# Kernel tuning notes

Measured on AMD Instinct MI355X. Metric: run time of the kernel, lower is better.

The kernel has to match this reference:

```python
import jax, jax.numpy as jnp
import numpy as np

N_NODES = 50000
N_EDGES = 600000
D = 128
EDGE_D = 32
N_LAYERS = 3
BN_EPS = 1e-5


def setup_inputs() -> dict:
    key = jax.random.key(0)
    ks = jax.random.split(key, 8)
    x = jax.random.normal(ks[0], (N_NODES, D), dtype=jnp.float32)
    edge_index = jax.random.randint(ks[1], (2, N_EDGES), 0, N_NODES, dtype=jnp.int64)
    edge_attr = jax.random.normal(ks[2], (N_EDGES, EDGE_D), dtype=jnp.float32)
    W_lin = jax.random.normal(ks[3], (N_LAYERS, EDGE_D, D), dtype=jnp.float32) * 0.05
    b_lin = jnp.zeros((N_LAYERS, D), dtype=jnp.float32)
    W1 = jax.random.normal(ks[4], (N_LAYERS, D, D), dtype=jnp.float32) * 0.05
    b1 = jnp.zeros((N_LAYERS, D), dtype=jnp.float32)
    W2 = jax.random.normal(ks[5], (N_LAYERS, D, D), dtype=jnp.float32) * 0.05
    b2 = jnp.zeros((N_LAYERS, D), dtype=jnp.float32)
    gamma = jnp.ones((N_LAYERS, D), dtype=jnp.float32)
    beta = jnp.zeros((N_LAYERS, D), dtype=jnp.float32)
    return {"x": x, "edge_index": edge_index, "edge_attr": edge_attr,
            "W_lin": W_lin, "b_lin": b_lin, "W1": W1, "b1": b1,
            "W2": W2, "b2": b2, "gamma": gamma, "beta": beta}


def reference(x, edge_index, edge_attr, W_lin, b_lin, W1, b1, W2, b2, gamma, beta):
    # MPNN with GINEConv layers: for each layer,
    #   msg_e = ReLU(x[src_e] + Linear(edge_attr_e))      (PyG GINEConv edge lift)
    #   agg_i = sum over edges with dst==i of msg_e        (scatter-sum)
    #   h     = MLP((1+eps)*x + agg), eps=0
    #   x     = ReLU(BatchNorm1d(h))                       (training-mode batch stats)
    src, dst = edge_index[0], edge_index[1]
    n = x.shape[0]
    for l in range(W1.shape[0]):
        e = edge_attr @ W_lin[l] + b_lin[l]                 # [E, D]
        msg = jax.nn.relu(x[src] + e)                       # gather + fuse
        agg = jax.ops.segment_sum(msg, dst, num_segments=n)  # [N, D]
        h = x + agg                                         # eps = 0
        h = jax.nn.relu(h @ W1[l] + b1[l]) @ W2[l] + b2[l]   # GIN MLP
        mu = jnp.mean(h, axis=0)
        var = jnp.var(h, axis=0)
        h = (h - mu) * jax.lax.rsqrt(var + BN_EPS) * gamma[l] + beta[l]
        x = jax.nn.relu(h)
    return x
```

## Files before the change

### kernel.cpp

```cpp
#include <hip/hip_runtime.h>

#define D_DIM 128
#define EDGE_DIM 32
#define BN_EPS 1e-5f

typedef __attribute__((ext_vector_type(8))) _Float16 f16x8;
typedef __attribute__((ext_vector_type(2))) _Float16 half2v;
typedef __attribute__((ext_vector_type(4))) float f32x4;
typedef unsigned short ushort_t;

__device__ __forceinline__ unsigned short f2h(float f) {
    union { _Float16 h; unsigned short u; } c;
    c.h = (_Float16)f;
    return c.u;
}
__device__ __forceinline__ unsigned pk2h(float lo, float hi) {
    return (unsigned)f2h(lo) | ((unsigned)f2h(hi) << 16);
}
__device__ __forceinline__ half2v asH2(unsigned u) {
    union { unsigned u; half2v h; } c;
    c.u = u;
    return c.h;
}
__device__ __forceinline__ float fdot2f(half2v a, half2v b, float c) {
#if __has_builtin(__builtin_amdgcn_fdot2)
    return __builtin_amdgcn_fdot2(a, b, c, false);
#else
    return c + (float)a.x * (float)b.x + (float)a.y * (float)b.y;
#endif
}

__global__ __launch_bounds__(256) void hist_kernel(
    const int* __restrict__ dst, int* __restrict__ cnt, int E)
{
    for (int e = blockIdx.x * 256 + threadIdx.x; e < E; e += gridDim.x * 256)
        atomicAdd(&cnt[dst[e]], 1);
}

__global__ __launch_bounds__(256) void scan_local_kernel(
    const int* __restrict__ cnt, int* __restrict__ off,
    int* __restrict__ blksum, int n)
{
    __shared__ int part[256];
    const int t = threadIdx.x;
    const int base = blockIdx.x * 2048 + t * 8;
    int v[8];
    int s = 0;
#pragma unroll
    for (int j = 0; j < 8; ++j) {
        const int idx = base + j;
        const int c = (idx < n) ? cnt[idx] : 0;
        v[j] = s;
        s += c;
    }
    part[t] = s;
    __syncthreads();
    for (int d = 1; d < 256; d <<= 1) {
        const int val = (t >= d) ? part[t - d] : 0;
        __syncthreads();
        part[t] += val;
        __syncthreads();
    }
    const int texcl = (t > 0) ? part[t - 1] : 0;
#pragma unroll
    for (int j = 0; j < 8; ++j) {
        const int idx = base + j;
        if (idx < n) off[idx] = texcl + v[j];
    }
    if (t == 255) blksum[blockIdx.x] = part[255];
}

__global__ __launch_bounds__(64) void scan_tops_kernel(
    int* __restrict__ blksum, int* __restrict__ off, int n, int B)
{
    if (threadIdx.x == 0) {
        int run = 0;
        for (int b = 0; b < B; ++b) {
            const int v = blksum[b];
            blksum[b] = run;
            run += v;
        }
        off[n] = run;
    }
}

__global__ __launch_bounds__(256) void scan_add_kernel(
    int* __restrict__ off, int* __restrict__ cur,
    const int* __restrict__ blksum, int n)
{
    const int base = blockIdx.x * 2048;
    const int add = blksum[blockIdx.x];
    for (int j = threadIdx.x; j < 2048; j += 256) {
        const int i = base + j;
        if (i < n) {
            const int v = off[i] + add;
            off[i] = v;
            cur[i] = v;
        }
    }
}

__global__ __launch_bounds__(256) void scatter_conv_kernel(
    const int* __restrict__ src, const int* __restrict__ dst,
    const float* __restrict__ ea,
    int* __restrict__ cur, int* __restrict__ srcs,
    uint4* __restrict__ ea16q, int E)
{
    for (int e = blockIdx.x * 256 + threadIdx.x; e < E; e += gridDim.x * 256) {
        const int p = atomicAdd(&cur[dst[e]], 1);
        srcs[p] = src[e];
        const float* __restrict__ er = ea + (size_t)e * EDGE_DIM;
#pragma unroll
        for (int q = 0; q < 4; ++q) {
            const float4 a = *(const float4*)(er + q * 8);
            const float4 b = *(const float4*)(er + q * 8 + 4);
            uint4 o;
            o.x = pk2h(a.x, a.y); o.y = pk2h(a.z, a.w);
            o.z = pk2h(b.x, b.y); o.w = pk2h(b.z, b.w);
            ea16q[(size_t)p * 4 + q] = o;
        }
    }
}

__global__ __launch_bounds__(256) void wbuild_kernel(
    const float* __restrict__ Wl, const float* __restrict__ W1f,
    const float* __restrict__ W2f,
    unsigned* __restrict__ wl16d, unsigned* __restrict__ wf1d,
    unsigned* __restrict__ wf2d)
{
    const int idx = blockIdx.x * 256 + threadIdx.x;
    if (idx < 2048) {
        const int kp = idx >> 7, c = idx & 127;
        wl16d[idx] = pk2h(Wl[(2 * kp) * D_DIM + c], Wl[(2 * kp + 1) * D_DIM + c]);
    } else if (idx < 10240) {
        const int i = idx - 2048;
        const int col = i >> 6, kp = i & 63;
        wf1d[i] = pk2h(W1f[(2 * kp) * D_DIM + col], W1f[(2 * kp + 1) * D_DIM + col]);
    } else if (idx < 18432) {
        const int i = idx - 10240;
        const int col = i >> 6, kp = i & 63;
        wf2d[i] = pk2h(W2f[(2 * kp) * D_DIM + col], W2f[(2 * kp + 1) * D_DIM + col]);
    }
}

__global__ __launch_bounds__(256) void xprep0_kernel(
    const float* __restrict__ h, uint2* __restrict__ x16q, int M)
{
    const int total = M * 32;
    for (int i = blockIdx.x * 256 + threadIdx.x; i < total; i += gridDim.x * 256) {
        const float4 v = ((const float4*)h)[i];
        uint2 o; o.x = pk2h(v.x, v.y); o.y = pk2h(v.z, v.w);
        x16q[i] = o;
    }
}

template<int OUTF32>
__global__ __launch_bounds__(256) void apply_kernel(
    const ushort_t* __restrict__ h16, const float* __restrict__ scsh,
    uint2* __restrict__ x16q, float* __restrict__ outp, int M)
{
    __shared__ float sc[128], sh[128];
    if (threadIdx.x < 128) {
        sc[threadIdx.x] = scsh[threadIdx.x];
        sh[threadIdx.x] = scsh[128 + threadIdx.x];
    }
    __syncthreads();
    const int total = M * 32;
    for (int i = blockIdx.x * 256 + threadIdx.x; i < total; i += gridDim.x * 256) {
        const uint2 hv = *(const uint2*)(h16 + (size_t)i * 4);
        const half2v a = asH2(hv.x), b = asH2(hv.y);
        const int c = (i & 31) * 4;
        const float v0 = fmaxf(fmaf((float)a.x, sc[c + 0], sh[c + 0]), 0.f);
        const float v1 = fmaxf(fmaf((float)a.y, sc[c + 1], sh[c + 1]), 0.f);
        const float v2 = fmaxf(fmaf((float)b.x, sc[c + 2], sh[c + 2]), 0.f);
        const float v3 = fmaxf(fmaf((float)b.y, sc[c + 3], sh[c + 3]), 0.f);
        if (OUTF32) {
            f32x4 o = {v0, v1, v2, v3};
            *(f32x4*)(outp + (size_t)i * 4) = o;
        } else {
            uint2 o; o.x = pk2h(v0, v1); o.y = pk2h(v2, v3);
            x16q[i] = o;
        }
    }
}

__global__ __launch_bounds__(256, 2) void edge_agg_kernel(
    const unsigned* __restrict__ x16d,
    const int*      __restrict__ srcs,
    const uint4*    __restrict__ ea16q,
    const int*      __restrict__ row_off,
    const unsigned* __restrict__ wl16d,
    const float*    __restrict__ bl,
    unsigned*       __restrict__ agg16d,
    int nNodes)
{
    const int lane = threadIdx.x & 63;
    const int wid  = threadIdx.x >> 6;

    unsigned wA[16], wB[16];
#pragma unroll
    for (int kp = 0; kp < 16; ++kp) {
        const uint2 w2 = *(const uint2*)(wl16d + kp * 128 + 2 * lane);
        wA[kp] = w2.x; wB[kp] = w2.y;
    }
#pragma unroll
    for (int kp = 0; kp < 16; ++kp) {
        asm volatile("" : "+v"(wA[kp]));
        asm volatile("" : "+v"(wB[kp]));
    }
    const float b0 = bl[2 * lane];
    const float b1 = bl[2 * lane + 1];

    const int stride = gridDim.x * 4;
    for (int node = blockIdx.x * 4 + wid; node < nNodes; node += stride) {
        const int beg = __builtin_amdgcn_readfirstlane(row_off[node]);
        const int end = __builtin_amdgcn_readfirstlane(row_off[node + 1]);
        float acc0 = 0.f, acc1 = 0.f;

        const int nPair = (end - beg) >> 1;
        int j = beg;
        int sA = 0, sB = 0;
        if (nPair > 0) { sA = srcs[j]; sB = srcs[j + 1]; }

#pragma unroll 1
        for (int it = 0; it < nPair; ++it) {
            const unsigned xdA = x16d[(size_t)sA * 64 + lane];
            const unsigned xdB = x16d[(size_t)sB * 64 + lane];
            int sA2 = sA, sB2 = sB;
            if (it + 1 < nPair) {
                sA2 = srcs[j + 2];
                sB2 = srcs[j + 3];
            }
            const uint4 a0 = ea16q[(size_t)j * 4 + 0];
            const uint4 a1 = ea16q[(size_t)j * 4 + 1];
            const uint4 a2 = ea16q[(size_t)j * 4 + 2];
            const uint4 a3 = ea16q[(size_t)j * 4 + 3];
            const uint4 c0 = ea16q[(size_t)(j + 1) * 4 + 0];
            const uint4 c1 = ea16q[(size_t)(j + 1) * 4 + 1];
            const uint4 c2 = ea16q[(size_t)(j + 1) * 4 + 2];
            const uint4 c3 = ea16q[(size_t)(j + 1) * 4 + 3];

            const unsigned awA[16] = {a0.x, a0.y, a0.z, a0.w,
                                      a1.x, a1.y, a1.z, a1.w,
                                      a2.x, a2.y, a2.z, a2.w,
                                      a3.x, a3.y, a3.z, a3.w};
            const unsigned awB[16] = {c0.x, c0.y, c0.z, c0.w,
                                      c1.x, c1.y, c1.z, c1.w,
                                      c2.x, c2.y, c2.z, c2.w,
                                      c3.x, c3.y, c3.z, c3.w};
            float pA0 = b0, pA1 = b1, pB0 = b0, pB1 = b1;
            float qA0 = 0.f, qA1 = 0.f, qB0 = 0.f, qB1 = 0.f;
#pragma unroll
            for (int kp = 0; kp < 8; ++kp) {
                pA0 = fdot2f(asH2(awA[kp]), asH2(wA[kp]), pA0);
                pA1 = fdot2f(asH2(awA[kp]), asH2(wB[kp]), pA1);
                pB0 = fdot2f(asH2(awB[kp]), asH2(wA[kp]), pB0);
                pB1 = fdot2f(asH2(awB[kp]), asH2(wB[kp]), pB1);
                qA0 = fdot2f(asH2(awA[kp + 8]), asH2(wA[kp + 8]), qA0);
                qA1 = fdot2f(asH2(awA[kp + 8]), asH2(wB[kp + 8]), qA1);
                qB0 = fdot2f(asH2(awB[kp + 8]), asH2(wA[kp + 8]), qB0);
                qB1 = fdot2f(asH2(awB[kp + 8]), asH2(wB[kp + 8]), qB1);
            }
            const half2v xhA = asH2(xdA);
            const half2v xhB = asH2(xdB);
            acc0 += fmaxf((float)xhA.x + pA0 + qA0, 0.f)
                  + fmaxf((float)xhB.x + pB0 + qB0, 0.f);
            acc1 += fmaxf((float)xhA.y + pA1 + qA1, 0.f)
                  + fmaxf((float)xhB.y + pB1 + qB1, 0.f);
            sA = sA2; sB = sB2;
            j += 2;
        }
        if (j < end) {
            const int s = srcs[j];
            const unsigned xd = x16d[(size_t)s * 64 + lane];
            const uint4 a0 = ea16q[(size_t)j * 4 + 0];
            const uint4 a1 = ea16q[(size_t)j * 4 + 1];
            const uint4 a2 = ea16q[(size_t)j * 4 + 2];
            const uint4 a3 = ea16q[(size_t)j * 4 + 3];
            const unsigned aw[16] = {a0.x, a0.y, a0.z, a0.w,
                                     a1.x, a1.y, a1.z, a1.w,
                                     a2.x, a2.y, a2.z, a2.w,
                                     a3.x, a3.y, a3.z, a3.w};
            float p0 = b0, p1 = b1, q0 = 0.f, q1 = 0.f;
#pragma unroll
            for (int kp = 0; kp < 8; ++kp) {
                p0 = fdot2f(asH2(aw[kp]), asH2(wA[kp]), p0);
                p1 = fdot2f(asH2(aw[kp]), asH2(wB[kp]), p1);
                q0 = fdot2f(asH2(aw[kp + 8]), asH2(wA[kp + 8]), q0);
                q1 = fdot2f(asH2(aw[kp + 8]), asH2(wB[kp + 8]), q1);
            }
            const half2v xh = asH2(xd);
            acc0 += fmaxf((float)xh.x + p0 + q0, 0.f);
            acc1 += fmaxf((float)xh.y + p1 + q1, 0.f);
        }
        const half2v xo = asH2(x16d[(size_t)node * 64 + lane]);
        agg16d[(size_t)node * 64 + lane] =
            pk2h((float)xo.x + acc0, (float)xo.y + acc1);
    }
}

__global__ __launch_bounds__(256) void fused_mlp_kernel(
    const unsigned* __restrict__ agg16d,
    const ushort_t* __restrict__ wf1,
    const float* __restrict__ b1,
    const ushort_t* __restrict__ wf2,
    const float* __restrict__ b2,
    ushort_t* __restrict__ h16,
    float* __restrict__ sums,
    int M)
{
    __shared__ char ATb[128 * 256];
    __shared__ float bsum[256];
    const int tid = threadIdx.x;
    const int m0  = blockIdx.x * 128;

    bsum[tid] = 0.f;

#pragma unroll
    for (int i = 0; i < 8; ++i) {
        const int idx = i * 256 + tid;
        const int r = idx >> 4, c16 = idx & 15;
        const int row = m0 + r;
        uint4 v = make_uint4(0u, 0u, 0u, 0u);
        if (row < M) v = *(const uint4*)(agg16d + (size_t)row * 64 + c16 * 4);
        *(uint4*)(ATb + r * 256 + ((c16 * 16) ^ ((r & 7) << 4))) = v;
    }
    __syncthreads();

    const int lane = tid & 63;
    const int w    = tid >> 6;
    const int fr   = lane & 15;
    const int fg   = lane >> 4;
    const int ar0  = w * 32 + fr;
    const int asz  = (ar0 & 7) << 4;

    f32x4 acc[2][8];
#pragma unroll
    for (int a = 0; a < 2; ++a)
#pragma unroll
        for (int b = 0; b < 8; ++b) acc[a][b] = (f32x4){0.f, 0.f, 0.f, 0.f};

#pragma unroll
    for (int ks = 0; ks < 4; ++ks) {
        const int kb = ks * 64 + fg * 16;
        const f16x8 a0 = *(const f16x8*)(ATb + ar0 * 256 + (kb ^ asz));
        const f16x8 a1 = *(const f16x8*)(ATb + (ar0 + 16) * 256 + (kb ^ asz));
        f16x8 bfr[8];
#pragma unroll
        for (int cb = 0; cb < 8; ++cb) {
            const int col = cb * 16 + fr;
            bfr[cb] = *(const f16x8*)(wf1 + col * 128 + ks * 32 + fg * 8);
        }
#pragma unroll
        for (int cb = 0; cb < 8; ++cb) {
            acc[0][cb] = __builtin_amdgcn_mfma_f32_16x16x32_f16(a0, bfr[cb], acc[0][cb], 0, 0, 0);
            acc[1][cb] = __builtin_amdgcn_mfma_f32_16x16x32_f16(a1, bfr[cb], acc[1][cb], 0, 0, 0);
        }
    }
    __syncthreads();

    {
        float b1v[8];
#pragma unroll
        for (int cb = 0; cb < 8; ++cb) b1v[cb] = b1[cb * 16 + fr];
#pragma unroll
        for (int rf = 0; rf < 2; ++rf) {
            const int rb = w * 32 + rf * 16 + fg * 4;
#pragma unroll
            for (int cb = 0; cb < 8; ++cb) {
                const int c = cb * 16 + fr;
#pragma unroll
                for (int j = 0; j < 4; ++j) {
                    const int r = rb + j;
                    const float v = fmaxf(acc[rf][cb][j] + b1v[cb], 0.f);
                    *(ushort_t*)(ATb + r * 256 + ((c * 2) ^ ((r & 7) << 4))) = f2h(v);
                }
            }
        }
    }
#pragma unroll
    for (int a = 0; a < 2; ++a)
#pragma unroll
        for (int b = 0; b < 8; ++b) acc[a][b] = (f32x4){0.f, 0.f, 0.f, 0.f};
    __syncthreads();

#pragma unroll
    for (int ks = 0; ks < 4; ++ks) {
        const int kb = ks * 64 + fg * 16;
        const f16x8 a0 = *(const f16x8*)(ATb + ar0 * 256 + (kb ^ asz));
        const f16x8 a1 = *(const f16x8*)(ATb + (ar0 + 16) * 256 + (kb ^ asz));
        f16x8 bfr[8];
#pragma unroll
        for (int cb = 0; cb < 8; ++cb) {
            const int col = cb * 16 + fr;
            bfr[cb] = *(const f16x8*)(wf2 + col * 128 + ks * 32 + fg * 8);
        }
#pragma unroll
        for (int cb = 0; cb < 8; ++cb) {
            acc[0][cb] = __builtin_amdgcn_mfma_f32_16x16x32_f16(a0, bfr[cb], acc[0][cb], 0, 0, 0);
            acc[1][cb] = __builtin_amdgcn_mfma_f32_16x16x32_f16(a1, bfr[cb], acc[1][cb], 0, 0, 0);
        }
    }

    float b2v[8];
#pragma unroll
    for (int cb = 0; cb < 8; ++cb) b2v[cb] = b2[cb * 16 + fr];
    float s[8], q[8];
#pragma unroll
    for (int cb = 0; cb < 8; ++cb) { s[cb] = 0.f; q[cb] = 0.f; }

#pragma unroll
    for (int rf = 0; rf < 2; ++rf) {
        const int r0 = m0 + w * 32 + rf * 16 + fg * 4;
#pragma unroll
        for (int cb = 0; cb < 8; ++cb) {
            const int col = cb * 16 + fr;
#pragma unroll
            for (int j = 0; j < 4; ++j) {
                const int row = r0 + j;
                if (row < M) {
                    const float v = acc[rf][cb][j] + b2v[cb];
                    h16[(size_t)row * 128 + col] = f2h(v);
                    s[cb] += v;
                    q[cb] += v * v;
                }
            }
        }
    }
#pragma unroll
    for (int cb = 0; cb < 8; ++cb) {
        float ss = s[cb]; ss += __shfl_down(ss, 32); ss += __shfl_down(ss, 16);
        float qq = q[cb]; qq += __shfl_down(qq, 32); qq += __shfl_down(qq, 16);
        if (lane < 16) {
            atomicAdd(&bsum[cb * 16 + lane], ss);
            atomicAdd(&bsum[128 + cb * 16 + lane], qq);
        }
    }
    __syncthreads();
    unsafeAtomicAdd(&sums[tid], bsum[tid]);
}

__global__ __launch_bounds__(128) void bn_finalize_kernel(
    const float* __restrict__ sums,
    const float* __restrict__ gamma, const float* __restrict__ beta,
    float* __restrict__ scsh, float invM)
{
    const int c = threadIdx.x;
    const float mu  = sums[c] * invM;
    const float var = sums[128 + c] * invM - mu * mu;
    const float sc  = gamma[c] * rsqrtf(var + BN_EPS);
    scsh[c]       = sc;
    scsh[128 + c] = beta[c] - mu * sc;
}

extern "C" void kernel_launch(void* const* d_in, const int* in_sizes, int n_in,
                              void* d_out, int out_size, void* d_ws, size_t ws_size,
                              hipStream_t stream)
{
    const float* x_in  = (const float*)d_in[0];
    const int*   ei    = (const int*)  d_in[1];
    const float* ea    = (const float*)d_in[2];
    const float* W_lin = (const float*)d_in[3];
    const float* b_lin = (const float*)d_in[4];
    const float* W1    = (const float*)d_in[5];
    const float* b1    = (const float*)d_in[6];
    const float* W2    = (const float*)d_in[7];
    const float* b2    = (const float*)d_in[8];
    const float* gamma = (const float*)d_in[9];
    const float* beta  = (const float*)d_in[10];

    const int N = in_sizes[0] / D_DIM;
    const int E = in_sizes[2] / EDGE_DIM;
    const int L = in_sizes[3] / (EDGE_DIM * D_DIM);

    const int* src = ei;
    const int* dst = ei + E;

    float* out = (float*)d_out;

    char* wp = (char*)d_ws;
    auto take = [&wp](size_t bytes) {
        char* r = wp;
        wp += (bytes + 15) & ~(size_t)15;
        return r;
    };
    unsigned*  agg16d  = (unsigned*) take((size_t)N * D_DIM * 2);
    ushort_t*  h16     = (ushort_t*) take((size_t)N * D_DIM * 2);
    unsigned*  x16d    = (unsigned*) take((size_t)N * D_DIM * 2);
    float*     sums    = (float*)    take(256 * 4);
    float*     scsh    = (float*)    take(256 * 4);
    unsigned*  wl16d   = (unsigned*) take(16 * 128 * 4);
    unsigned*  wf1d    = (unsigned*) take(128 * 64 * 4);
    unsigned*  wf2d    = (unsigned*) take(128 * 64 * 4);
    int*       cnt     = (int*)      take((size_t)N * 4);
    int*       row_off = (int*)      take((size_t)(N + 1) * 4);
    int*       cur     = (int*)      take((size_t)N * 4);
    int*       blksum  = (int*)      take(256 * 4);
    int*       srcs    = (int*)      take((size_t)E * 4);
    uint4*     ea16q   = (uint4*)    take((size_t)E * 64);

    const int gemmBlocks = (N + 127) / 128;
    const int scanBlocks = (N + 2047) / 2048;

    hipMemsetAsync(cnt, 0, (size_t)N * sizeof(int), stream);
    hist_kernel<<<1024, 256, 0, stream>>>(dst, cnt, E);
    scan_local_kernel<<<scanBlocks, 256, 0, stream>>>(cnt, row_off, blksum, N);
    scan_tops_kernel<<<1, 64, 0, stream>>>(blksum, row_off, N, scanBlocks);
    scan_add_kernel<<<scanBlocks, 256, 0, stream>>>(row_off, cur, blksum, N);
    scatter_conv_kernel<<<1024, 256, 0, stream>>>(src, dst, ea, cur, srcs, ea16q, E);

    for (int l = 0; l < L; ++l) {
        hipMemsetAsync(sums, 0, 256 * sizeof(float), stream);

        const float* Wl_l = W_lin + (size_t)l * EDGE_DIM * D_DIM;
        const float* bl_l = b_lin + (size_t)l * D_DIM;
        const float* W1_l = W1 + (size_t)l * D_DIM * D_DIM;
        const float* b1_l = b1 + (size_t)l * D_DIM;
        const float* W2_l = W2 + (size_t)l * D_DIM * D_DIM;
        const float* b2_l = b2 + (size_t)l * D_DIM;

        if (l == 0)
            xprep0_kernel<<<1024, 256, 0, stream>>>(x_in, (uint2*)x16d, N);
        else
            apply_kernel<0><<<1024, 256, 0, stream>>>(h16, scsh, (uint2*)x16d, nullptr, N);

        wbuild_kernel<<<72, 256, 0, stream>>>(Wl_l, W1_l, W2_l, wl16d, wf1d, wf2d);

        edge_agg_kernel<<<2048, 256, 0, stream>>>(
            x16d, srcs, ea16q, row_off, wl16d, bl_l, agg16d, N);

        fused_mlp_kernel<<<gemmBlocks, 256, 0, stream>>>(
            agg16d, (const ushort_t*)wf1d, b1_l,
            (const ushort_t*)wf2d, b2_l, h16, sums, N);

        bn_finalize_kernel<<<1, 128, 0, stream>>>(
            sums, gamma + (size_t)l * D_DIM, beta + (size_t)l * D_DIM,
            scsh, 1.f / (float)N);
    }

    apply_kernel<1><<<1024, 256, 0, stream>>>(h16, scsh, nullptr, out, N);
}
```

Baseline: 439.3 us.

## Fuse BatchNorm apply into edge aggregation and hoist per-layer weight conversion

The BN finalize and apply kernels between layers are removed. Each edge_agg launch now computes the scale and shift from the accumulated sums and applies the normalisation plus ReLU on the fly to every gathered source row and to the self term, reading the fp16 MLP output directly. All three layers' weights are converted in one kernel up front and the stats buffers are zeroed once, which cuts the number of kernel launches and memsets. The cost is repeated per-edge normalisation arithmetic inside the gather loop (about 12 edges per node) in place of one elementwise pass over the nodes.

Result: faster. 420.1 us (-4.4%).

```diff
diff --git a/kernel.cpp b/kernel.cpp
--- a/kernel.cpp
+++ b/kernel.cpp
@@ -122,24 +122,30 @@
     }
 }
 
-__global__ __launch_bounds__(256) void wbuild_kernel(
-    const float* __restrict__ Wl, const float* __restrict__ W1f,
-    const float* __restrict__ W2f,
-    unsigned* __restrict__ wl16d, unsigned* __restrict__ wf1d,
-    unsigned* __restrict__ wf2d)
+__global__ __launch_bounds__(256) void wbuild_all_kernel(
+    const float* __restrict__ W_lin, const float* __restrict__ W1,
+    const float* __restrict__ W2,
+    unsigned* __restrict__ wl3, unsigned* __restrict__ wf13,
+    unsigned* __restrict__ wf23)
 {
     const int idx = blockIdx.x * 256 + threadIdx.x;
-    if (idx < 2048) {
-        const int kp = idx >> 7, c = idx & 127;
-        wl16d[idx] = pk2h(Wl[(2 * kp) * D_DIM + c], Wl[(2 * kp + 1) * D_DIM + c]);
-    } else if (idx < 10240) {
-        const int i = idx - 2048;
+    if (idx >= 3 * 18432) return;
+    const int l = idx / 18432;
+    const int r = idx % 18432;
+    const float* Wl  = W_lin + (size_t)l * EDGE_DIM * D_DIM;
+    const float* W1l = W1 + (size_t)l * D_DIM * D_DIM;
+    const float* W2l = W2 + (size_t)l * D_DIM * D_DIM;
+    if (r < 2048) {
+        const int kp = r >> 7, c = r & 127;
+        wl3[l * 2048 + r] = pk2h(Wl[(2 * kp) * D_DIM + c], Wl[(2 * kp + 1) * D_DIM + c]);
+    } else if (r < 10240) {
+        const int i = r - 2048;
         const int col = i >> 6, kp = i & 63;
-        wf1d[i] = pk2h(W1f[(2 * kp) * D_DIM + col], W1f[(2 * kp + 1) * D_DIM + col]);
-    } else if (idx < 18432) {
-        const int i = idx - 10240;
+        wf13[l * 8192 + i] = pk2h(W1l[(2 * kp) * D_DIM + col], W1l[(2 * kp + 1) * D_DIM + col]);
+    } else {
+        const int i = r - 10240;
         const int col = i >> 6, kp = i & 63;
-        wf2d[i] = pk2h(W2f[(2 * kp) * D_DIM + col], W2f[(2 * kp + 1) * D_DIM + col]);
+        wf23[l * 8192 + i] = pk2h(W2l[(2 * kp) * D_DIM + col], W2l[(2 * kp + 1) * D_DIM + col]);
     }
 }
 
@@ -154,15 +160,19 @@
     }
 }
 
-template<int OUTF32>
-__global__ __launch_bounds__(256) void apply_kernel(
-    const ushort_t* __restrict__ h16, const float* __restrict__ scsh,
-    uint2* __restrict__ x16q, float* __restrict__ outp, int M)
+__global__ __launch_bounds__(256) void apply_final_kernel(
+    const ushort_t* __restrict__ h16, const float* __restrict__ sums,
+    const float* __restrict__ gamma, const float* __restrict__ beta,
+    float invN, float* __restrict__ outp, int M)
 {
     __shared__ float sc[128], sh[128];
     if (threadIdx.x < 128) {
-        sc[threadIdx.x] = scsh[threadIdx.x];
-        sh[threadIdx.x] = scsh[128 + threadIdx.x];
+        const int c = threadIdx.x;
+        const float mu  = sums[c] * invN;
+        const float var = sums[128 + c] * invN - mu * mu;
+        const float s   = gamma[c] * rsqrtf(var + BN_EPS);
+        sc[c] = s;
+        sh[c] = beta[c] - mu * s;
     }
     __syncthreads();
     const int total = M * 32;
@@ -170,27 +180,27 @@
         const uint2 hv = *(const uint2*)(h16 + (size_t)i * 4);
         const half2v a = asH2(hv.x), b = asH2(hv.y);
         const int c = (i & 31) * 4;
-        const float v0 = fmaxf(fmaf((float)a.x, sc[c + 0], sh[c + 0]), 0.f);
-        const float v1 = fmaxf(fmaf((float)a.y, sc[c + 1], sh[c + 1]), 0.f);
-        const float v2 = fmaxf(fmaf((float)b.x, sc[c + 2], sh[c + 2]), 0.f);
-        const float v3 = fmaxf(fmaf((float)b.y, sc[c + 3], sh[c + 3]), 0.f);
-        if (OUTF32) {
-            f32x4 o = {v0, v1, v2, v3};
-            *(f32x4*)(outp + (size_t)i * 4) = o;
-        } else {
-            uint2 o; o.x = pk2h(v0, v1); o.y = pk2h(v2, v3);
-            x16q[i] = o;
-        }
-    }
-}
-
+        f32x4 o;
+        o[0] = fmaxf(fmaf((float)a.x, sc[c + 0], sh[c + 0]), 0.f);
+        o[1] = fmaxf(fmaf((float)a.y, sc[c + 1], sh[c + 1]), 0.f);
+        o[2] = fmaxf(fmaf((float)b.x, sc[c + 2], sh[c + 2]), 0.f);
+        o[3] = fmaxf(fmaf((float)b.y, sc[c + 3], sh[c + 3]), 0.f);
+        *(f32x4*)(outp + (size_t)i * 4) = o;
+    }
+}
+
+template<int XFORM>
 __global__ __launch_bounds__(256, 2) void edge_agg_kernel(
-    const unsigned* __restrict__ x16d,
+    const unsigned* __restrict__ hsrc,
     const int*      __restrict__ srcs,
     const uint4*    __restrict__ ea16q,
     const int*      __restrict__ row_off,
     const unsigned* __restrict__ wl16d,
     const float*    __restrict__ bl,
+    const float*    __restrict__ sums,
+    const float*    __restrict__ gamma,
+    const float*    __restrict__ beta,
+    float invN,
     unsigned*       __restrict__ agg16d,
     int nNodes)
 {
@@ -210,6 +220,19 @@
     }
     const float b0 = bl[2 * lane];
     const float b1 = bl[2 * lane + 1];
+
+    float scl0 = 1.f, shl0 = 0.f, scl1 = 1.f, shl1 = 0.f;
+    if (XFORM) {
+        const int c0 = 2 * lane, c1 = 2 * lane + 1;
+        const float mu0 = sums[c0] * invN;
+        const float va0 = sums[128 + c0] * invN - mu0 * mu0;
+        scl0 = gamma[c0] * rsqrtf(va0 + BN_EPS);
+        shl0 = beta[c0] - mu0 * scl0;
+        const float mu1 = sums[c1] * invN;
+        const float va1 = sums[128 + c1] * invN - mu1 * mu1;
+        scl1 = gamma[c1] * rsqrtf(va1 + BN_EPS);
+        shl1 = beta[c1] - mu1 * scl1;
+    }
 
     const int stride = gridDim.x * 4;
     for (int node = blockIdx.x * 4 + wid; node < nNodes; node += stride) {
@@ -224,8 +247,8 @@
 
 #pragma unroll 1
         for (int it = 0; it < nPair; ++it) {
-            const unsigned xdA = x16d[(size_t)sA * 64 + lane];
-            const unsigned xdB = x16d[(size_t)sB * 64 + lane];
+            const unsigned xdA = hsrc[(size_t)sA * 64 + lane];
+            const unsigned xdB = hsrc[(size_t)sB * 64 + lane];
             int sA2 = sA, sB2 = sB;
             if (it + 1 < nPair) {
                 sA2 = srcs[j + 2];
@@ -263,16 +286,22 @@
             }
             const half2v xhA = asH2(xdA);
             const half2v xhB = asH2(xdB);
-            acc0 += fmaxf((float)xhA.x + pA0 + qA0, 0.f)
-                  + fmaxf((float)xhB.x + pB0 + qB0, 0.f);
-            acc1 += fmaxf((float)xhA.y + pA1 + qA1, 0.f)
-                  + fmaxf((float)xhB.y + pB1 + qB1, 0.f);
+            float xA0 = (float)xhA.x, xA1 = (float)xhA.y;
+            float xB0 = (float)xhB.x, xB1 = (float)xhB.y;
+            if (XFORM) {
+                xA0 = fmaxf(fmaf(xA0, scl0, shl0), 0.f);
+                xA1 = fmaxf(fmaf(xA1, scl1, shl1), 0.f);
+                xB0 = fmaxf(fmaf(xB0, scl0, shl0), 0.f);
+                xB1 = fmaxf(fmaf(xB1, scl1, shl1), 0.f);
+            }
+            acc0 += fmaxf(xA0 + pA0 + qA0, 0.f) + fmaxf(xB0 + pB0 + qB0, 0.f);
+            acc1 += fmaxf(xA1 + pA1 + qA1, 0.f) + fmaxf(xB1 + pB1 + qB1, 0.f);
             sA = sA2; sB = sB2;
             j += 2;
         }
         if (j < end) {
             const int s = srcs[j];
-            const unsigned xd = x16d[(size_t)s * 64 + lane];
+            const unsigned xd = hsrc[(size_t)s * 64 + lane];
             const uint4 a0 = ea16q[(size_t)j * 4 + 0];
             const uint4 a1 = ea16q[(size_t)j * 4 + 1];
             const uint4 a2 = ea16q[(size_t)j * 4 + 2];
@@ -290,12 +319,21 @@
                 q1 = fdot2f(asH2(aw[kp + 8]), asH2(wB[kp + 8]), q1);
             }
             const half2v xh = asH2(xd);
-            acc0 += fmaxf((float)xh.x + p0 + q0, 0.f);
-            acc1 += fmaxf((float)xh.y + p1 + q1, 0.f);
-        }
-        const half2v xo = asH2(x16d[(size_t)node * 64 + lane]);
-        agg16d[(size_t)node * 64 + lane] =
-            pk2h((float)xo.x + acc0, (float)xo.y + acc1);
+            float x0 = (float)xh.x, x1 = (float)xh.y;
+            if (XFORM) {
+                x0 = fmaxf(fmaf(x0, scl0, shl0), 0.f);
+                x1 = fmaxf(fmaf(x1, scl1, shl1), 0.f);
+            }
+            acc0 += fmaxf(x0 + p0 + q0, 0.f);
+            acc1 += fmaxf(x1 + p1 + q1, 0.f);
+        }
+        const half2v xo = asH2(hsrc[(size_t)node * 64 + lane]);
+        float x0 = (float)xo.x, x1 = (float)xo.y;
+        if (XFORM) {
+            x0 = fmaxf(fmaf(x0, scl0, shl0), 0.f);
+            x1 = fmaxf(fmaf(x1, scl1, shl1), 0.f);
+        }
+        agg16d[(size_t)node * 64 + lane] = pk2h(x0 + acc0, x1 + acc1);
     }
 }
 
@@ -345,16 +383,14 @@
         const int kb = ks * 64 + fg * 16;
         const f16x8 a0 = *(const f16x8*)(ATb + ar0 * 256 + (kb ^ asz));
         const f16x8 a1 = *(const f16x8*)(ATb + (ar0 + 16) * 256 + (kb ^ asz));
-        f16x8 bfr[8];
+        f16x8 bf[8];
+#pragma unroll
+        for (int cb = 0; cb < 8; ++cb)
+            bf[cb] = *(const f16x8*)(wf1 + (cb * 16 + fr) * 128 + ks * 32 + fg * 8);
 #pragma unroll
         for (int cb = 0; cb < 8; ++cb) {
-            const int col = cb * 16 + fr;
-            bfr[cb] = *(const f16x8*)(wf1 + col * 128 + ks * 32 + fg * 8);
-        }
-#pragma unroll
-        for (int cb = 0; cb < 8; ++cb) {
-            acc[0][cb] = __builtin_amdgcn_mfma_f32_16x16x32_f16(a0, bfr[cb], acc[0][cb], 0, 0, 0);
-            acc[1][cb] = __builtin_amdgcn_mfma_f32_16x16x32_f16(a1, bfr[cb], acc[1][cb], 0, 0, 0);
+            acc[0][cb] = __builtin_amdgcn_mfma_f32_16x16x32_f16(a0, bf[cb], acc[0][cb], 0, 0, 0);
+            acc[1][cb] = __builtin_amdgcn_mfma_f32_16x16x32_f16(a1, bf[cb], acc[1][cb], 0, 0, 0);
         }
     }
     __syncthreads();
@@ -368,12 +404,12 @@
             const int rb = w * 32 + rf * 16 + fg * 4;
 #pragma unroll
             for (int cb = 0; cb < 8; ++cb) {
-                const int c = cb * 16 + fr;
+                const int cc = cb * 16 + fr;
 #pragma unroll
                 for (int j = 0; j < 4; ++j) {
                     const int r = rb + j;
                     const float v = fmaxf(acc[rf][cb][j] + b1v[cb], 0.f);
-                    *(ushort_t*)(ATb + r * 256 + ((c * 2) ^ ((r & 7) << 4))) = f2h(v);
+                    *(ushort_t*)(ATb + r * 256 + ((cc * 2) ^ ((r & 7) << 4))) = f2h(v);
                 }
             }
         }
@@ -389,16 +425,14 @@
         const int kb = ks * 64 + fg * 16;
         const f16x8 a0 = *(const f16x8*)(ATb + ar0 * 256 + (kb ^ asz));
         const f16x8 a1 = *(const f16x8*)(ATb + (ar0 + 16) * 256 + (kb ^ asz));
-        f16x8 bfr[8];
+        f16x8 bf[8];
+#pragma unroll
+        for (int cb = 0; cb < 8; ++cb)
+            bf[cb] = *(const f16x8*)(wf2 + (cb * 16 + fr) * 128 + ks * 32 + fg * 8);
 #pragma unroll
         for (int cb = 0; cb < 8; ++cb) {
-            const int col = cb * 16 + fr;
-            bfr[cb] = *(const f16x8*)(wf2 + col * 128 + ks * 32 + fg * 8);
-        }
-#pragma unroll
-        for (int cb = 0; cb < 8; ++cb) {
-            acc[0][cb] = __builtin_amdgcn_mfma_f32_16x16x32_f16(a0, bfr[cb], acc[0][cb], 0, 0, 0);
-            acc[1][cb] = __builtin_amdgcn_mfma_f32_16x16x32_f16(a1, bfr[cb], acc[1][cb], 0, 0, 0);
+            acc[0][cb] = __builtin_amdgcn_mfma_f32_16x16x32_f16(a0, bf[cb], acc[0][cb], 0, 0, 0);
+            acc[1][cb] = __builtin_amdgcn_mfma_f32_16x16x32_f16(a1, bf[cb], acc[1][cb], 0, 0, 0);
         }
     }
 
@@ -438,19 +472,6 @@
     }
     __syncthreads();
     unsafeAtomicAdd(&sums[tid], bsum[tid]);
-}
-
-__global__ __launch_bounds__(128) void bn_finalize_kernel(
-    const float* __restrict__ sums,
-    const float* __restrict__ gamma, const float* __restrict__ beta,
-    float* __restrict__ scsh, float invM)
-{
-    const int c = threadIdx.x;
-    const float mu  = sums[c] * invM;
-    const float var = sums[128 + c] * invM - mu * mu;
-    const float sc  = gamma[c] * rsqrtf(var + BN_EPS);
-    scsh[c]       = sc;
-    scsh[128 + c] = beta[c] - mu * sc;
 }
 
 extern "C" void kernel_launch(void* const* d_in, const int* in_sizes, int n_in,
@@ -472,6 +493,7 @@
     const int N = in_sizes[0] / D_DIM;
     const int E = in_sizes[2] / EDGE_DIM;
     const int L = in_sizes[3] / (EDGE_DIM * D_DIM);
+    const float invN = 1.f / (float)N;
 
     const int* src = ei;
     const int* dst = ei + E;
@@ -487,11 +509,10 @@
     unsigned*  agg16d  = (unsigned*) take((size_t)N * D_DIM * 2);
     ushort_t*  h16     = (ushort_t*) take((size_t)N * D_DIM * 2);
     unsigned*  x16d    = (unsigned*) take((size_t)N * D_DIM * 2);
-    float*     sums    = (float*)    take(256 * 4);
-    float*     scsh    = (float*)    take(256 * 4);
-    unsigned*  wl16d   = (unsigned*) take(16 * 128 * 4);
-    unsigned*  wf1d    = (unsigned*) take(128 * 64 * 4);
-    unsigned*  wf2d    = (unsigned*) take(128 * 64 * 4);
+    float*     sums3   = (float*)    take(3 * 256 * 4);
+    unsigned*  wl3     = (unsigned*) take(3 * 2048 * 4);
+    unsigned*  wf13    = (unsigned*) take(3 * 8192 * 4);
+    unsigned*  wf23    = (unsigned*) take(3 * 8192 * 4);
     int*       cnt     = (int*)      take((size_t)N * 4);
     int*       row_off = (int*)      take((size_t)(N + 1) * 4);
     int*       cur     = (int*)      take((size_t)N * 4);
@@ -503,40 +524,41 @@
     const int scanBlocks = (N + 2047) / 2048;
 
     hipMemsetAsync(cnt, 0, (size_t)N * sizeof(int), stream);
+    hipMemsetAsync(sums3, 0, 3 * 256 * sizeof(float), stream);
     hist_kernel<<<1024, 256, 0, stream>>>(dst, cnt, E);
     scan_local_kernel<<<scanBlocks, 256, 0, stream>>>(cnt, row_off, blksum, N);
     scan_tops_kernel<<<1, 64, 0, stream>>>(blksum, row_off, N, scanBlocks);
     scan_add_kernel<<<scanBlocks, 256, 0, stream>>>(row_off, cur, blksum, N);
     scatter_conv_kernel<<<1024, 256, 0, stream>>>(src, dst, ea, cur, srcs, ea16q, E);
+    wbuild_all_kernel<<<216, 256, 0, stream>>>(W_lin, W1, W2, wl3, wf13, wf23);
+    xprep0_kernel<<<1024, 256, 0, stream>>>(x_in, (uint2*)x16d, N);
 
     for (int l = 0; l < L; ++l) {
-        hipMemsetAsync(sums, 0, 256 * sizeof(float), stream);
-
-        const float* Wl_l = W_lin + (size_t)l * EDGE_DIM * D_DIM;
         const float* bl_l = b_lin + (size_t)l * D_DIM;
-        const float* W1_l = W1 + (size_t)l * D_DIM * D_DIM;
         const float* b1_l = b1 + (size_t)l * D_DIM;
-        const float* W2_l = W2 + (size_t)l * D_DIM * D_DIM;
         const float* b2_l = b2 + (size_t)l * D_DIM;
-
-        if (l == 0)
-            xprep0_kernel<<<1024, 256, 0, stream>>>(x_in, (uint2*)x16d, N);
-        else
-            apply_kernel<0><<<1024, 256, 0, stream>>>(h16, scsh, (uint2*)x16d, nullptr, N);
-
-        wbuild_kernel<<<72, 256, 0, stream>>>(Wl_l, W1_l, W2_l, wl16d, wf1d, wf2d);
-
-        edge_agg_kernel<<<2048, 256, 0, stream>>>(
-            x16d, srcs, ea16q, row_off, wl16d, bl_l, agg16d, N);
+        const unsigned* wl_l = wl3 + (size_t)l * 2048;
+        const ushort_t* wf1_l = (const ushort_t*)(wf13 + (size_t)l * 8192);
+        const ushort_t* wf2_l = (const ushort_t*)(wf23 + (size_t)l * 8192);
+
+        if (l == 0) {
+            edge_agg_kernel<0><<<2048, 256, 0, stream>>>(
+                x16d, srcs, ea16q, row_off, wl_l, bl_l,
+                nullptr, nullptr, nullptr, invN, agg16d, N);
+        } else {
+            edge_agg_kernel<1><<<2048, 256, 0, stream>>>(
+                (const unsigned*)h16, srcs, ea16q, row_off, wl_l, bl_l,
+                sums3 + (size_t)(l - 1) * 256,
+                gamma + (size_t)(l - 1) * D_DIM,
+                beta + (size_t)(l - 1) * D_DIM, invN, agg16d, N);
+        }
 
         fused_mlp_kernel<<<gemmBlocks, 256, 0, stream>>>(
-            agg16d, (const ushort_t*)wf1d, b1_l,
-            (const ushort_t*)wf2d, b2_l, h16, sums, N);
-
-        bn_finalize_kernel<<<1, 128, 0, stream>>>(
-            sums, gamma + (size_t)l * D_DIM, beta + (size_t)l * D_DIM,
-            scsh, 1.f / (float)N);
-    }
-
-    apply_kernel<1><<<1024, 256, 0, stream>>>(h16, scsh, nullptr, out, N);
-}
+            agg16d, wf1_l, b1_l, wf2_l, b2_l, h16,
+            sums3 + (size_t)l * 256, N);
+    }
+
+    apply_final_kernel<<<1024, 256, 0, stream>>>(
+        h16, sums3 + 2 * 256, gamma + 2 * D_DIM, beta + 2 * D_DIM,
+        invN, out, N);
+}
```
